# Optimization experiments

Hardware: AMD Instinct MI355X
Metric: run time of the kernel (lower is better)

## Reference

```python
import jax, jax.numpy as jnp
import numpy as np
from jax import lax

B, C, H, W, E = 16, 256, 64, 64, 4
KH = KW = 3
EPS = 1e-5  # torch BatchNorm2d default


def conv2d(x, w, groups=1):
    # x: [N, Cin, H, W], w: [Cout, Cin/groups, KH, KW], stride 1, pad 1 (autopad for k=3)
    return lax.conv_general_dilated(
        x, w, window_strides=(1, 1), padding=[(1, 1), (1, 1)],
        dimension_numbers=('NCHW', 'OIHW', 'NCHW'),
        feature_group_count=groups)


def bn(t, g, b, m, v):
    # eval-mode batchnorm over channel dim of [N, C, H, W]
    scale = g / jnp.sqrt(v + EPS)
    return (t - m[:, None, None]) * scale[:, None, None] + b[:, None, None]


def silu(t):
    return t * jax.nn.sigmoid(t)


def setup_inputs() -> dict:
    key = jax.random.key(0)
    ks = jax.random.split(key, 8)
    s = lambda k, sh: jax.random.normal(k, sh, jnp.float32) * 0.05
    return {
        'x': jax.random.normal(ks[0], (B, C, H, W), jnp.float32),
        # cv1: Conv(c1, c_, 3) = conv(no bias) + BN + SiLU
        'w1': s(ks[1], (C, C, KH, KW)),
        'bn1_g': jnp.ones((C,), jnp.float32),
        'bn1_b': jnp.zeros((C,), jnp.float32),
        'bn1_m': s(ks[2], (C,)),
        'bn1_v': jnp.abs(s(ks[3], (C,))) + 1.0,
        # cv2: DynamicConv routing linear (C -> E experts)
        'wr': s(ks[4], (E, C)),
        'br': jnp.zeros((E,), jnp.float32),
        # CondConv2d expert weight bank: [E, Cout*Cin*KH*KW]
        'w_e': s(ks[5], (E, C * C * KH * KW)),
        # cv2 BatchNorm2d
        'bn2_g': jnp.ones((C,), jnp.float32),
        'bn2_b': jnp.zeros((C,), jnp.float32),
        'bn2_m': s(ks[6], (C,)),
        'bn2_v': jnp.abs(s(ks[7], (C,))) + 1.0,
    }


def reference(x, w1, bn1_g, bn1_b, bn1_m, bn1_v, wr, br, w_e,
              bn2_g, bn2_b, bn2_m, bn2_v):
    # cv1: standard YOLO Conv (3x3, pad 1) + BN + SiLU
    y = silu(bn(conv2d(x, w1), bn1_g, bn1_b, bn1_m, bn1_v))  # [B, C, H, W]

    # DynamicConv_Single: global-avg-pool routing -> sigmoid gates over experts
    pooled = y.mean(axis=(2, 3))                       # [B, C]
    routing = jax.nn.sigmoid(pooled @ wr.T + br)       # [B, E]

    # CondConv2d: per-sample expert-weighted kernel, applied via batch-as-groups
    kern = (routing @ w_e).reshape(B * C, C, KH, KW)   # [B*Cout, Cin, 3, 3]
    yc = conv2d(y.reshape(1, B * C, H, W), kern, groups=B).reshape(B, C, H, W)

    # cv2 BN + SiLU, then residual add (shortcut and c1 == c2)
    out = silu(bn(yc, bn2_g, bn2_b, bn2_m, bn2_v))
    return x + out


if __name__ == '__main__':
    o = reference(**setup_inputs())
    print(o.shape, o.dtype)
```

## Files before the change

### kernel.cpp

```cpp
#include <hip/hip_runtime.h>
#include <math.h>

typedef _Float16 h16;
typedef _Float16 half8 __attribute__((ext_vector_type(8)));
typedef float f32x4 __attribute__((ext_vector_type(4)));

#define BATCH 16
#define CH 256
#define EPSBN 1e-5f

constexpr size_t WE_STRIDE = (size_t)CH * CH * 9;
constexpr int REG = 2120;

__device__ __forceinline__ float silu_(float v) {
    return v * (1.0f / (1.0f + __expf(-v)));
}

template<int MODE>
__global__ __launch_bounds__(256, 3)
void conv_mfma(const h16* __restrict__ xin,
               const h16* __restrict__ wt,
               const float* __restrict__ bng, const float* __restrict__ bnb,
               const float* __restrict__ bnm, const float* __restrict__ bnv,
               const float* __restrict__ resid,
               void* __restrict__ outv)
{
    __shared__ h16 xt[4 * REG];

    const int t    = threadIdx.x;
    const int bx   = blockIdx.x;
    const int by   = blockIdx.y;
    const int bz   = blockIdx.z;
    const int h0   = bx * 2;
    const int co0  = by * 128;
    const int wv   = t >> 6;
    const int lane = t & 63;
    const int quad = lane >> 4;
    const int l15  = lane & 15;

    f32x4 acc[16];
    #pragma unroll
    for (int i = 0; i < 16; ++i) {
        f32x4 z = {0.f, 0.f, 0.f, 0.f};
        acc[i] = z;
    }

    const h16* wrow = wt + ((MODE == 1) ? (size_t)bz * 9 * 65536 : (size_t)0)
                         + ((size_t)(co0 + wv * 32 + l15) << 8)
                         + (size_t)(quad * 8);
    const h16* xlane = xt + quad * REG + l15 * 8;

    for (int ci0 = 0; ci0 < CH; ci0 += 32) {
        __syncthreads();
        #pragma unroll
        for (int k = 0; k < 5; ++k) {
            int idx = t + k * 256;
            if (idx < 1056) {
                int cig = idx & 3;
                int sp  = idx >> 2;
                int row = sp / 66;
                int col = sp - row * 66;
                int gh = h0 - 1 + row, gw = col - 1;
                half8 v = {0, 0, 0, 0, 0, 0, 0, 0};
                if ((unsigned)gh < 64u && (unsigned)gw < 64u)
                    v = *(const half8*)(xin + (((size_t)(bz * 64 + gh) << 6) + gw) * 256
                                            + ci0 + cig * 8);
                *(half8*)(xt + cig * REG + sp * 8) = v;
            }
        }
        __syncthreads();

        const h16* wc = wrow + ci0;
        #pragma unroll
        for (int kh = 0; kh < 3; ++kh)
        #pragma unroll
        for (int kw = 0; kw < 3; ++kw) {
            const int tap = kh * 3 + kw;
            half8 wf[2], xf[8];
            #pragma unroll
            for (int f = 0; f < 2; ++f)
                wf[f] = *(const half8*)(wc + (size_t)tap * 65536 + f * 4096);
            #pragma unroll
            for (int i = 0; i < 8; ++i)
                xf[i] = *(const half8*)(xlane + ((kh + (i >> 2)) * 66 + (i & 3) * 16 + kw) * 8);
            if (MODE == 0) {
                #pragma unroll
                for (int i = 0; i < 8; ++i)
                    #pragma unroll
                    for (int j = 0; j < 2; ++j)
                        acc[i * 2 + j] = __builtin_amdgcn_mfma_f32_16x16x32_f16(
                            xf[i], wf[j], acc[i * 2 + j], 0, 0, 0);
            } else {
                #pragma unroll
                for (int i = 0; i < 2; ++i)
                    #pragma unroll
                    for (int j = 0; j < 8; ++j)
                        acc[i * 8 + j] = __builtin_amdgcn_mfma_f32_16x16x32_f16(
                            wf[i], xf[j], acc[i * 8 + j], 0, 0, 0);
            }
        }
    }

    if (MODE == 0) {
        h16* yout = (h16*)outv;
        float sc[2], sh[2];
        #pragma unroll
        for (int j = 0; j < 2; ++j) {
            int c = co0 + wv * 32 + j * 16 + l15;
            float s = bng[c] * rsqrtf(bnv[c] + EPSBN);
            sc[j] = s; sh[j] = bnb[c] - bnm[c] * s;
        }
        #pragma unroll
        for (int i = 0; i < 8; ++i)
            #pragma unroll
            for (int r = 0; r < 4; ++r) {
                int spL = i * 16 + quad * 4 + r;
                int h = h0 + (spL >> 6), w = spL & 63;
                size_t base = (((size_t)(bz * 64 + h) << 6) + w) * 256
                            + co0 + wv * 32 + l15;
                #pragma unroll
                for (int j = 0; j < 2; ++j) {
                    float v = acc[i * 2 + j][r] * sc[j] + sh[j];
                    yout[base + j * 16] = (h16)silu_(v);
                }
            }
    } else {
        float* outp = (float*)outv;
        #pragma unroll
        for (int i = 0; i < 2; ++i) {
            float sc[4], sh[4];
            #pragma unroll
            for (int r = 0; r < 4; ++r) {
                int c = co0 + wv * 32 + i * 16 + quad * 4 + r;
                float s = bng[c] * rsqrtf(bnv[c] + EPSBN);
                sc[r] = s; sh[r] = bnb[c] - bnm[c] * s;
            }
            #pragma unroll
            for (int j = 0; j < 8; ++j) {
                int spL = j * 16 + l15;
                int h = h0 + (spL >> 6), w = spL & 63;
                #pragma unroll
                for (int r = 0; r < 4; ++r) {
                    int c = co0 + wv * 32 + i * 16 + quad * 4 + r;
                    size_t idx = ((size_t)(bz * CH + c) << 12) + (h << 6) + w;
                    float v = acc[i * 8 + j][r] * sc[r] + sh[r];
                    outp[idx] = resid[idx] + silu_(v);
                }
            }
        }
    }
}

__global__ __launch_bounds__(256)
void prep_x(const float* __restrict__ x, h16* __restrict__ xh) {
    __shared__ float lt[64][65];
    int cg = blockIdx.x, h = blockIdx.y, b = blockIdx.z;
    int t = threadIdx.x;
    {
        int cl = t >> 2, wq = t & 3;
        const float4* src = (const float4*)(x + (((size_t)(b * CH + cg * 64 + cl)) << 12)
                                              + ((size_t)h << 6));
        #pragma unroll
        for (int k = 0; k < 4; ++k) {
            int w4 = wq + k * 4;
            float4 v = src[w4];
            lt[cl][w4 * 4 + 0] = v.x;
            lt[cl][w4 * 4 + 1] = v.y;
            lt[cl][w4 * 4 + 2] = v.z;
            lt[cl][w4 * 4 + 3] = v.w;
        }
    }
    __syncthreads();
    {
        int wl = t >> 2, cq = t & 3;
        half8 a2[2];
        h16* ap = (h16*)a2;
        #pragma unroll
        for (int m = 0; m < 16; ++m) ap[m] = (h16)lt[cq * 16 + m][wl];
        size_t base = ((((size_t)(b * 64 + h)) << 6) + wl) * 256 + cg * 64 + cq * 16;
        *(half8*)(xh + base)     = a2[0];
        *(half8*)(xh + base + 8) = a2[1];
    }
}

__global__ void prep_w1(const float* __restrict__ w1, h16* __restrict__ w1t) {
    int pair = blockIdx.x * 256 + threadIdx.x;
    #pragma unroll
    for (int tap = 0; tap < 9; ++tap)
        w1t[((size_t)tap << 16) + pair] = (h16)w1[(size_t)pair * 9 + tap];
}

__global__ __launch_bounds__(256)
void pool_kernel(const h16* __restrict__ y, float* __restrict__ part) {
    __shared__ float red[8][256];
    int slice = blockIdx.x, b = blockIdx.y;
    int t = threadIdx.x;
    int oct = t & 31, ss = t >> 5;
    float a[8];
    #pragma unroll
    for (int k = 0; k < 8; ++k) a[k] = 0.f;
    const h16* p = y + ((size_t)(b * 4096 + slice * 256 + ss)) * 256 + oct * 8;
    #pragma unroll 4
    for (int i = 0; i < 32; ++i) {
        half8 v = *(const half8*)(p + (size_t)i * 8 * 256);
        #pragma unroll
        for (int k = 0; k < 8; ++k) a[k] += (float)v[k];
    }
    #pragma unroll
    for (int k = 0; k < 8; ++k) red[ss][oct * 8 + k] = a[k];
    __syncthreads();
    float s = 0.f;
    #pragma unroll
    for (int q = 0; q < 8; ++q) s += red[q][t];
    part[((size_t)slice * BATCH + b) * 256 + t] = s;
}

__global__ void routing_kernel(const float* __restrict__ part,
                               const float* __restrict__ wr,
                               const float* __restrict__ br,
                               float* __restrict__ routing) {
    int t = threadIdx.x;
    if (t < 64) {
        int b = t >> 2, e = t & 3;
        float s = 0.f;
        for (int c = 0; c < 256; ++c) {
            float p = 0.f;
            for (int sl = 0; sl < 16; ++sl)
                p += part[((size_t)sl * BATCH + b) * 256 + c];
            s += p * wr[e * 256 + c];
        }
        s = s * (1.f / 4096.f) + br[e];
        routing[t] = 1.f / (1.f + __expf(-s));
    }
}

__global__ __launch_bounds__(256)
void kern_gen(const float* __restrict__ w_e,
              const float* __restrict__ routing,
              h16* __restrict__ wt2) {
    __shared__ float lw[4 * 2304];
    __shared__ float rsh[64];
    int t = threadIdx.x;
    int pair0 = blockIdx.x * 256;
    if (t < 64) rsh[t] = routing[t];
    #pragma unroll
    for (int e = 0; e < 4; ++e) {
        const float4* src = (const float4*)(w_e + (size_t)e * WE_STRIDE + (size_t)pair0 * 9);
        #pragma unroll
        for (int k = 0; k < 3; ++k) {
            int idx = t + k * 256;
            if (idx < 576) {
                float4 v = src[idx];
                float* d = &lw[e * 2304 + idx * 4];
                d[0] = v.x; d[1] = v.y; d[2] = v.z; d[3] = v.w;
            }
        }
    }
    __syncthreads();
    float wv[4][9];
    #pragma unroll
    for (int e = 0; e < 4; ++e)
        #pragma unroll
        for (int k = 0; k < 9; ++k)
            wv[e][k] = lw[e * 2304 + t * 9 + k];
    for (int b = 0; b < 16; ++b) {
        float r0 = rsh[b * 4 + 0], r1 = rsh[b * 4 + 1];
        float r2 = rsh[b * 4 + 2], r3 = rsh[b * 4 + 3];
        #pragma unroll
        for (int tap = 0; tap < 9; ++tap) {
            float s = r0 * wv[0][tap] + r1 * wv[1][tap]
                    + r2 * wv[2][tap] + r3 * wv[3][tap];
            wt2[((size_t)(b * 9 + tap) << 16) + pair0 + t] = (h16)s;
        }
    }
}

extern "C" void kernel_launch(void* const* d_in, const int* in_sizes, int n_in,
                              void* d_out, int out_size, void* d_ws, size_t ws_size,
                              hipStream_t stream) {
    const float* x    = (const float*)d_in[0];
    const float* w1   = (const float*)d_in[1];
    const float* bn1g = (const float*)d_in[2];
    const float* bn1b = (const float*)d_in[3];
    const float* bn1m = (const float*)d_in[4];
    const float* bn1v = (const float*)d_in[5];
    const float* wr   = (const float*)d_in[6];
    const float* br   = (const float*)d_in[7];
    const float* w_e  = (const float*)d_in[8];
    const float* bn2g = (const float*)d_in[9];
    const float* bn2b = (const float*)d_in[10];
    const float* bn2m = (const float*)d_in[11];
    const float* bn2v = (const float*)d_in[12];

    char* w = (char*)d_ws;
    h16*   xh      = (h16*)(w);
    h16*   y       = (h16*)(w + 33554432);
    h16*   w1t     = (h16*)(w + 67108864);
    h16*   wt2     = (h16*)(w + 68288512);
    float* part    = (float*)(w + 87162880);
    float* routing = (float*)(w + 87425024);

    prep_x<<<dim3(4, 64, BATCH), 256, 0, stream>>>(x, xh);
    prep_w1<<<dim3(256), 256, 0, stream>>>(w1, w1t);

    dim3 cgrid(32, 2, BATCH);
    conv_mfma<0><<<cgrid, 256, 0, stream>>>(xh, w1t, bn1g, bn1b, bn1m, bn1v,
                                            nullptr, y);
    pool_kernel<<<dim3(16, BATCH), 256, 0, stream>>>(y, part);
    routing_kernel<<<dim3(1), 64, 0, stream>>>(part, wr, br, routing);
    kern_gen<<<dim3(256), 256, 0, stream>>>(w_e, routing, wt2);
    conv_mfma<1><<<cgrid, 256, 0, stream>>>(y, wt2, bn2g, bn2b, bn2m, bn2v,
                                            x, (float*)d_out);
}
```

Before: 479.1 us.

## Double-buffer input tiles in LDS with register prefetch and swizzled block order

The conv kernel now double-buffers its LDS input tile. It issues the global loads for the next 32-channel chunk into registers before computing the current chunk, then stores them into the alternate buffer, so only one barrier is needed per chunk. Global addresses for the tile are precomputed once outside the loop. The grid is flattened to 1D with a block-index swizzle that changes which (row, cout-half, batch) tiles run concurrently, likely to improve L2 reuse. The cost is double the LDS and extra registers for prefetch and pointers, which may lower occupancy.

Measured after the change: 490.6 us. 1.02x slower.

```diff
diff --git a/kernel.cpp b/kernel.cpp
--- a/kernel.cpp
+++ b/kernel.cpp
@@ -10,7 +10,8 @@
 #define EPSBN 1e-5f
 
 constexpr size_t WE_STRIDE = (size_t)CH * CH * 9;
-constexpr int REG = 2120;
+constexpr int REG  = 2120;
+constexpr int BUFH = 4 * REG;
 
 __device__ __forceinline__ float silu_(float v) {
     return v * (1.0f / (1.0f + __expf(-v)));
@@ -25,14 +26,16 @@
                const float* __restrict__ resid,
                void* __restrict__ outv)
 {
-    __shared__ h16 xt[4 * REG];
-
-    const int t    = threadIdx.x;
-    const int bx   = blockIdx.x;
-    const int by   = blockIdx.y;
-    const int bz   = blockIdx.z;
-    const int h0   = bx * 2;
-    const int co0  = by * 128;
+    __shared__ h16 xt[2 * BUFH];
+
+    const int t = threadIdx.x;
+    const int swz = (blockIdx.x & 7) * 128 + (blockIdx.x >> 3);
+    const int bx  = swz & 31;
+    const int gy  = swz >> 5;
+    const int by  = gy & 1;
+    const int bz  = gy >> 1;
+    const int h0  = bx * 2;
+    const int co0 = by * 128;
     const int wv   = t >> 6;
     const int lane = t & 63;
     const int quad = lane >> 4;
@@ -48,29 +51,29 @@
     const h16* wrow = wt + ((MODE == 1) ? (size_t)bz * 9 * 65536 : (size_t)0)
                          + ((size_t)(co0 + wv * 32 + l15) << 8)
                          + (size_t)(quad * 8);
-    const h16* xlane = xt + quad * REG + l15 * 8;
-
-    for (int ci0 = 0; ci0 < CH; ci0 += 32) {
-        __syncthreads();
-        #pragma unroll
-        for (int k = 0; k < 5; ++k) {
-            int idx = t + k * 256;
-            if (idx < 1056) {
-                int cig = idx & 3;
-                int sp  = idx >> 2;
-                int row = sp / 66;
-                int col = sp - row * 66;
-                int gh = h0 - 1 + row, gw = col - 1;
-                half8 v = {0, 0, 0, 0, 0, 0, 0, 0};
-                if ((unsigned)gh < 64u && (unsigned)gw < 64u)
-                    v = *(const half8*)(xin + (((size_t)(bz * 64 + gh) << 6) + gw) * 256
-                                            + ci0 + cig * 8);
-                *(half8*)(xt + cig * REG + sp * 8) = v;
-            }
-        }
-        __syncthreads();
-
-        const h16* wc = wrow + ci0;
+
+    const h16* gptr[5];
+    int lofs[5];
+    #pragma unroll
+    for (int k = 0; k < 5; ++k) {
+        int idx = t + k * 256;
+        gptr[k] = nullptr;
+        lofs[k] = -1;
+        if (idx < 1056) {
+            int cig = idx & 3;
+            int sp  = idx >> 2;
+            int row = sp / 66;
+            int col = sp - row * 66;
+            int gh = h0 - 1 + row, gw = col - 1;
+            lofs[k] = cig * REG + sp * 8;
+            if ((unsigned)gh < 64u && (unsigned)gw < 64u)
+                gptr[k] = xin + (((size_t)(bz * 64 + gh) << 6) + gw) * 256 + cig * 8;
+        }
+    }
+
+    auto compute_chunk = [&](int c) {
+        const h16* xb = xt + (c & 1) * BUFH + quad * REG + l15 * 8;
+        const h16* wc = wrow + c * 32;
         #pragma unroll
         for (int kh = 0; kh < 3; ++kh)
         #pragma unroll
@@ -82,7 +85,7 @@
                 wf[f] = *(const half8*)(wc + (size_t)tap * 65536 + f * 4096);
             #pragma unroll
             for (int i = 0; i < 8; ++i)
-                xf[i] = *(const half8*)(xlane + ((kh + (i >> 2)) * 66 + (i & 3) * 16 + kw) * 8);
+                xf[i] = *(const half8*)(xb + ((kh + (i >> 2)) * 66 + (i & 3) * 16 + kw) * 8);
             if (MODE == 0) {
                 #pragma unroll
                 for (int i = 0; i < 8; ++i)
@@ -99,7 +102,36 @@
                             wf[i], xf[j], acc[i * 8 + j], 0, 0, 0);
             }
         }
-    }
+    };
+
+    {
+        half8 r[5];
+        #pragma unroll
+        for (int k = 0; k < 5; ++k) {
+            half8 z = {0, 0, 0, 0, 0, 0, 0, 0};
+            r[k] = gptr[k] ? *(const half8*)(gptr[k]) : z;
+        }
+        #pragma unroll
+        for (int k = 0; k < 5; ++k)
+            if (lofs[k] >= 0) *(half8*)(xt + lofs[k]) = r[k];
+    }
+    __syncthreads();
+
+    for (int c = 0; c < 7; ++c) {
+        half8 r[5];
+        #pragma unroll
+        for (int k = 0; k < 5; ++k) {
+            half8 z = {0, 0, 0, 0, 0, 0, 0, 0};
+            r[k] = gptr[k] ? *(const half8*)(gptr[k] + (c + 1) * 32) : z;
+        }
+        compute_chunk(c);
+        #pragma unroll
+        for (int k = 0; k < 5; ++k)
+            if (lofs[k] >= 0)
+                *(half8*)(xt + ((c + 1) & 1) * BUFH + lofs[k]) = r[k];
+        __syncthreads();
+    }
+    compute_chunk(7);
 
     if (MODE == 0) {
         h16* yout = (h16*)outv;
@@ -303,7 +335,7 @@
     prep_x<<<dim3(4, 64, BATCH), 256, 0, stream>>>(x, xh);
     prep_w1<<<dim3(256), 256, 0, stream>>>(w1, w1t);
 
-    dim3 cgrid(32, 2, BATCH);
+    dim3 cgrid(1024);
     conv_mfma<0><<<cgrid, 256, 0, stream>>>(xh, w1t, bn1g, bn1b, bn1m, bn1v,
                                             nullptr, y);
     pool_kernel<<<dim3(16, BATCH), 256, 0, stream>>>(y, part);
```

## Retile conv waves to 2x2 spatial/channel split with block swizzle and hoisted load offsets

Applied to the files above, without the earlier changes.

Each wave now computes one spatial row by 64 output channels (a 4x4 MFMA tile) instead of two rows by 32 channels (8x2). This balances A/B fragment loads, with 8 loads per 16 MFMAs instead of 10. The grid is flattened to 1D with a swizzle so that consecutive blocks map to different batches and rows, aiming for better cache and XCD distribution. Halo-load index math is precomputed once outside the channel loop, and the launch bound now targets 4 blocks per CU, which adds register pressure from the precomputed offsets.

New measurement: 533.8 us. +11.4%, slower.

```diff
diff --git a/kernel.cpp b/kernel.cpp
--- a/kernel.cpp
+++ b/kernel.cpp
@@ -17,7 +17,7 @@
 }
 
 template<int MODE>
-__global__ __launch_bounds__(256, 3)
+__global__ __launch_bounds__(256, 4)
 void conv_mfma(const h16* __restrict__ xin,
                const h16* __restrict__ wt,
                const float* __restrict__ bng, const float* __restrict__ bnb,
@@ -27,13 +27,17 @@
 {
     __shared__ h16 xt[4 * REG];
 
-    const int t    = threadIdx.x;
-    const int bx   = blockIdx.x;
-    const int by   = blockIdx.y;
-    const int bz   = blockIdx.z;
-    const int h0   = bx * 2;
-    const int co0  = by * 128;
+    const int t = threadIdx.x;
+    const int swz = (blockIdx.x & 7) * 128 + (blockIdx.x >> 3);
+    const int bx  = swz & 31;
+    const int gy  = swz >> 5;
+    const int by  = gy & 1;
+    const int bz  = gy >> 1;
+    const int h0  = bx * 2;
+    const int co0 = by * 128;
     const int wv   = t >> 6;
+    const int ws   = wv >> 1;
+    const int wc   = wv & 1;
     const int lane = t & 63;
     const int quad = lane >> 4;
     const int l15  = lane & 15;
@@ -46,104 +50,117 @@
     }
 
     const h16* wrow = wt + ((MODE == 1) ? (size_t)bz * 9 * 65536 : (size_t)0)
-                         + ((size_t)(co0 + wv * 32 + l15) << 8)
+                         + ((size_t)(co0 + wc * 64 + l15) << 8)
                          + (size_t)(quad * 8);
+
+    const h16* xb = xin + ((size_t)bz << 20);
+    int goff[5], lofs[5];
+    #pragma unroll
+    for (int k = 0; k < 5; ++k) {
+        int idx = t + k * 256;
+        goff[k] = -1;
+        lofs[k] = -1;
+        if (idx < 1056) {
+            int cig = idx & 3;
+            int sp  = idx >> 2;
+            int row = sp / 66;
+            int col = sp - row * 66;
+            int gh = h0 - 1 + row, gw = col - 1;
+            lofs[k] = cig * REG + sp * 8;
+            if ((unsigned)gh < 64u && (unsigned)gw < 64u)
+                goff[k] = ((gh << 6) + gw) * 256 + cig * 8;
+        }
+    }
+
     const h16* xlane = xt + quad * REG + l15 * 8;
 
-    for (int ci0 = 0; ci0 < CH; ci0 += 32) {
+    for (int c = 0; c < 8; ++c) {
+        const int ci0 = c * 32;
         __syncthreads();
         #pragma unroll
         for (int k = 0; k < 5; ++k) {
-            int idx = t + k * 256;
-            if (idx < 1056) {
-                int cig = idx & 3;
-                int sp  = idx >> 2;
-                int row = sp / 66;
-                int col = sp - row * 66;
-                int gh = h0 - 1 + row, gw = col - 1;
+            if (lofs[k] >= 0) {
                 half8 v = {0, 0, 0, 0, 0, 0, 0, 0};
-                if ((unsigned)gh < 64u && (unsigned)gw < 64u)
-                    v = *(const half8*)(xin + (((size_t)(bz * 64 + gh) << 6) + gw) * 256
-                                            + ci0 + cig * 8);
-                *(half8*)(xt + cig * REG + sp * 8) = v;
+                if (goff[k] >= 0) v = *(const half8*)(xb + goff[k] + ci0);
+                *(half8*)(xt + lofs[k]) = v;
             }
         }
         __syncthreads();
 
-        const h16* wc = wrow + ci0;
+        const h16* wcp = wrow + ci0;
         #pragma unroll
         for (int kh = 0; kh < 3; ++kh)
         #pragma unroll
         for (int kw = 0; kw < 3; ++kw) {
             const int tap = kh * 3 + kw;
-            half8 wf[2], xf[8];
-            #pragma unroll
-            for (int f = 0; f < 2; ++f)
-                wf[f] = *(const half8*)(wc + (size_t)tap * 65536 + f * 4096);
-            #pragma unroll
-            for (int i = 0; i < 8; ++i)
-                xf[i] = *(const half8*)(xlane + ((kh + (i >> 2)) * 66 + (i & 3) * 16 + kw) * 8);
+            half8 wf[4], xf[4];
+            #pragma unroll
+            for (int f = 0; f < 4; ++f)
+                wf[f] = *(const half8*)(wcp + (size_t)tap * 65536 + f * 4096);
+            #pragma unroll
+            for (int i = 0; i < 4; ++i)
+                xf[i] = *(const half8*)(xlane + ((ws + kh) * 66 + i * 16 + kw) * 8);
             if (MODE == 0) {
                 #pragma unroll
-                for (int i = 0; i < 8; ++i)
+                for (int i = 0; i < 4; ++i)
                     #pragma unroll
-                    for (int j = 0; j < 2; ++j)
-                        acc[i * 2 + j] = __builtin_amdgcn_mfma_f32_16x16x32_f16(
-                            xf[i], wf[j], acc[i * 2 + j], 0, 0, 0);
+                    for (int j = 0; j < 4; ++j)
+                        acc[i * 4 + j] = __builtin_amdgcn_mfma_f32_16x16x32_f16(
+                            xf[i], wf[j], acc[i * 4 + j], 0, 0, 0);
             } else {
                 #pragma unroll
-                for (int i = 0; i < 2; ++i)
+                for (int i = 0; i < 4; ++i)
                     #pragma unroll
-                    for (int j = 0; j < 8; ++j)
-                        acc[i * 8 + j] = __builtin_amdgcn_mfma_f32_16x16x32_f16(
-                            wf[i], xf[j], acc[i * 8 + j], 0, 0, 0);
+                    for (int j = 0; j < 4; ++j)
+                        acc[i * 4 + j] = __builtin_amdgcn_mfma_f32_16x16x32_f16(
+                            wf[i], xf[j], acc[i * 4 + j], 0, 0, 0);
             }
         }
     }
 
     if (MODE == 0) {
         h16* yout = (h16*)outv;
-        float sc[2], sh[2];
-        #pragma unroll
-        for (int j = 0; j < 2; ++j) {
-            int c = co0 + wv * 32 + j * 16 + l15;
-            float s = bng[c] * rsqrtf(bnv[c] + EPSBN);
-            sc[j] = s; sh[j] = bnb[c] - bnm[c] * s;
-        }
-        #pragma unroll
-        for (int i = 0; i < 8; ++i)
+        float sc[4], sh[4];
+        #pragma unroll
+        for (int j = 0; j < 4; ++j) {
+            int cch = co0 + wc * 64 + j * 16 + l15;
+            float s = bng[cch] * rsqrtf(bnv[cch] + EPSBN);
+            sc[j] = s; sh[j] = bnb[cch] - bnm[cch] * s;
+        }
+        const int h = h0 + ws;
+        #pragma unroll
+        for (int i = 0; i < 4; ++i)
             #pragma unroll
             for (int r = 0; r < 4; ++r) {
-                int spL = i * 16 + quad * 4 + r;
-                int h = h0 + (spL >> 6), w = spL & 63;
+                int w = i * 16 + quad * 4 + r;
                 size_t base = (((size_t)(bz * 64 + h) << 6) + w) * 256
-                            + co0 + wv * 32 + l15;
+                            + co0 + wc * 64 + l15;
                 #pragma unroll
-                for (int j = 0; j < 2; ++j) {
-                    float v = acc[i * 2 + j][r] * sc[j] + sh[j];
+                for (int j = 0; j < 4; ++j) {
+                    float v = acc[i * 4 + j][r] * sc[j] + sh[j];
                     yout[base + j * 16] = (h16)silu_(v);
                 }
             }
     } else {
         float* outp = (float*)outv;
-        #pragma unroll
-        for (int i = 0; i < 2; ++i) {
+        const int h = h0 + ws;
+        #pragma unroll
+        for (int i = 0; i < 4; ++i) {
             float sc[4], sh[4];
             #pragma unroll
             for (int r = 0; r < 4; ++r) {
-                int c = co0 + wv * 32 + i * 16 + quad * 4 + r;
-                float s = bng[c] * rsqrtf(bnv[c] + EPSBN);
-                sc[r] = s; sh[r] = bnb[c] - bnm[c] * s;
-            }
-            #pragma unroll
-            for (int j = 0; j < 8; ++j) {
-                int spL = j * 16 + l15;
-                int h = h0 + (spL >> 6), w = spL & 63;
+                int cch = co0 + wc * 64 + i * 16 + quad * 4 + r;
+                float s = bng[cch] * rsqrtf(bnv[cch] + EPSBN);
+                sc[r] = s; sh[r] = bnb[cch] - bnm[cch] * s;
+            }
+            #pragma unroll
+            for (int j = 0; j < 4; ++j) {
+                int w = j * 16 + l15;
                 #pragma unroll
                 for (int r = 0; r < 4; ++r) {
-                    int c = co0 + wv * 32 + i * 16 + quad * 4 + r;
-                    size_t idx = ((size_t)(bz * CH + c) << 12) + (h << 6) + w;
-                    float v = acc[i * 8 + j][r] * sc[r] + sh[r];
+                    int cch = co0 + wc * 64 + i * 16 + quad * 4 + r;
+                    size_t idx = ((size_t)(bz * CH + cch) << 12) + (h << 6) + w;
+                    float v = acc[i * 4 + j][r] * sc[r] + sh[r];
                     outp[idx] = resid[idx] + silu_(v);
                 }
             }
@@ -303,7 +320,7 @@
     prep_x<<<dim3(4, 64, BATCH), 256, 0, stream>>>(x, xh);
     prep_w1<<<dim3(256), 256, 0, stream>>>(w1, w1t);
 
-    dim3 cgrid(32, 2, BATCH);
+    dim3 cgrid(1024);
     conv_mfma<0><<<cgrid, 256, 0, stream>>>(xh, w1t, bn1g, bn1b, bn1m, bn1v,
                                             nullptr, y);
     pool_kernel<<<dim3(16, BATCH), 256, 0, stream>>>(y, part);
```
